# Optimization experiments

Hardware: AMD Instinct MI355X
Metric: run time of the kernel (lower is better)

## Reference

```python
import jax, jax.numpy as jnp
import numpy as np

BETA = 8.0  # cfg.memory.beta (inverse temperature)
EPS = 1e-12  # matches F.normalize default eps


def _l2_normalize(x):
    return x / jnp.maximum(jnp.linalg.norm(x, axis=-1, keepdims=True), EPS)


def setup_inputs() -> dict:
    key = jax.random.key(0)
    k1, k2, k3 = jax.random.split(key, 3)
    embeddings = jax.random.normal(k1, (1024, 128), dtype=jnp.float32)   # queries [B, D]
    keys = jax.random.normal(k2, (100000, 128), dtype=jnp.float32)       # stored patterns [N, D]
    labels = jax.random.randint(k3, (100000,), 0, 1000)                  # class per stored pattern [N]
    return {"embeddings": embeddings, "keys": keys, "labels": labels, "n_classes": 1000}


def reference(embeddings, keys, labels, n_classes):
    # store(): keys normalized (normalize_keys=True); values = one_hot(labels)
    k = _l2_normalize(keys)
    # query(): normalize queries, cosine sims, softmax(beta*sims), weighted value sum
    q = _l2_normalize(embeddings)
    sims = q @ k.T                                   # [B, N]
    weights = jax.nn.softmax(BETA * sims, axis=-1)   # [B, N]
    # weights @ one_hot(labels, C) == segment-sum of weights by key label (same math,
    # avoids materializing the dense [N, C] one-hot value matrix)
    out = jax.ops.segment_sum(weights.T, labels, num_segments=n_classes).T  # [B, C]
    return out
```

## Files before the change

kernel.cpp:

```cpp
#include <hip/hip_runtime.h>
#include <math.h>

typedef _Float16 f16;
typedef _Float16 f16x8 __attribute__((ext_vector_type(8)));
typedef float    f32x16 __attribute__((ext_vector_type(16)));
typedef unsigned int uint;
typedef unsigned short u16;

#define B_Q     1024
#define DIM     128
#define N_KEYS  100000
#define NPAD    102400
#define NGP     (NPAD / 32)
#define GPC     8
#define NCHUNK  (NGP / GPC)
#define N_CLS   1000
#define QSCALE  11.541560327111707f
#define CSUM    10
#define NCB     (N_CLS / CSUM)
#define NH      128

__global__ void k_hist(const int* __restrict__ labels, uint* __restrict__ hist128) {
    __shared__ uint lh[N_CLS];
    for (int i = threadIdx.x; i < N_CLS; i += blockDim.x) lh[i] = 0;
    __syncthreads();
    const int stride = gridDim.x * blockDim.x;
    for (int i = blockIdx.x * blockDim.x + threadIdx.x; i < N_KEYS; i += stride)
        atomicAdd(&lh[labels[i]], 1u);
    __syncthreads();
    for (int i = threadIdx.x; i < N_CLS; i += blockDim.x)
        hist128[blockIdx.x * N_CLS + i] = lh[i];
}

__global__ void k_scan(const uint* __restrict__ hist128, uint* __restrict__ cursor) {
    __shared__ uint s[1024];
    const int t = threadIdx.x;
    uint v = 0;
    if (t < N_CLS)
        for (int b = 0; b < NH; ++b) v += hist128[b * N_CLS + t];
    s[t] = v; __syncthreads();
    for (int o = 1; o < 1024; o <<= 1) {
        const uint x = (t >= o) ? s[t - o] : 0u;
        __syncthreads();
        s[t] += x;
        __syncthreads();
    }
    if (t < N_CLS) cursor[t] = s[t] - v;
}

__global__ void k_prep(const float* __restrict__ qm, const float* __restrict__ km,
                       const int* __restrict__ labels, uint* __restrict__ cursor,
                       f16* __restrict__ kf2, f16* __restrict__ qf2,
                       u16* __restrict__ kcls) {
    const int gid  = blockIdx.x * blockDim.x + threadIdx.x;
    const int n    = gid >> 6;
    const int lane = threadIdx.x & 63;
    if (n >= NPAD + B_Q) return;
    const bool isq   = n >= NPAD;
    const bool dummy = !isq && n >= N_KEYS;

    float a = 0.0f, b = 0.0f;
    if (!dummy) {
        const float* row = isq ? qm + (size_t)(n - NPAD) * DIM
                               : km + (size_t)n * DIM;
        a = row[lane]; b = row[lane + 64];
    }
    float ss = a * a + b * b;
    #pragma unroll
    for (int o = 32; o >= 1; o >>= 1) ss += __shfl_xor(ss, o);
    const float rn = (isq ? QSCALE : 1.0f) / fmaxf(sqrtf(ss), 1e-12f);

    int pos;
    if (isq)        pos = n - NPAD;
    else if (dummy) { pos = n; if (lane == 0) kcls[pos] = (u16)N_CLS; }
    else {
        const int lab = labels[n];
        if (lane == 0) pos = (int)atomicAdd(&cursor[lab], 1u);
        pos = __shfl(pos, 0);
        if (lane == 0) kcls[pos] = (u16)lab;
    }

    const float va = a * rn, vb = b * rn;
    f16x8 hv;
    #pragma unroll
    for (int j = 0; j < 8; ++j) {
        const int src = (lane & 15) * 8 + j;
        const float xa = __shfl(va, src & 63);
        const float xb = __shfl(vb, src & 63);
        hv[j] = (f16)((src < 64) ? xa : xb);
    }
    if (lane < 16) {
        f16* dst = isq ? qf2 : kf2;
        const int kk  = lane >> 1;
        const int lhi = lane & 1;
        *(f16x8*)(dst + (size_t)(pos >> 5) * 4096 + kk * 512 +
                  ((lhi << 5) + (pos & 31)) * 8) = hv;
    }
}

__global__ void k_meta(const u16* __restrict__ kcls, int* __restrict__ meta,
                       float* __restrict__ out_t) {
    const int nt = gridDim.x * blockDim.x;
    const float4 z = {0.0f, 0.0f, 0.0f, 0.0f};
    for (int i = blockIdx.x * blockDim.x + threadIdx.x;
         i < N_CLS * B_Q / 4; i += nt)
        ((float4*)out_t)[i] = z;

    const int gid  = blockIdx.x * blockDim.x + threadIdx.x;
    const int g    = gid >> 6;
    const int lane = threadIdx.x & 63;
    if (g >= NGP) return;
    const int  cl = kcls[g * 32 + (lane & 31)];
    const int  ca = __shfl(cl, 0);
    const uint dm = (uint)(__ballot(cl != ca) & 0xffffffffull);
    const int  split = dm ? (__ffs(dm) - 1) : 32;
    const int  cb = (split < 32) ? __shfl(cl, split) : ca;
    if (lane == 0) meta[g] = ca | (cb << 11) | (split << 22);
}

#define FLUSH2(C) {                                                           \
        const float v0 = racc0 + __shfl_xor(racc0, 32);                       \
        const float v1 = racc1 + __shfl_xor(racc1, 32);                       \
        if (lhi == 0) {                                                       \
            atomicAdd(&out_t[(size_t)(C) * B_Q + q00 + l31], v0);             \
            atomicAdd(&out_t[(size_t)(C) * B_Q + q01 + l31], v1);             \
        }                                                                     \
    }

__global__ __launch_bounds__(256, 3)
void class_gemm6(const f16* __restrict__ kf2, const f16* __restrict__ qf2,
                 const int* __restrict__ meta, float* __restrict__ out_t) {
    const int tid  = threadIdx.x;
    const int w    = tid >> 6;
    const int lane = tid & 63;
    const int l31  = lane & 31;
    const int lhi  = lane >> 5;
    const int lhi4 = lhi << 2;

    const int b     = blockIdx.x;
    const int xcd   = b & 7;
    const int s     = b >> 3;
    const int chunk = xcd * (NCHUNK / 8) + (s >> 2);
    const int qquad = s & 3;
    const int g0    = chunk * GPC;

    f16x8 Q0[8], Q1[8];
    {
        const f16* qa = qf2 + (size_t)(qquad * 8 + w * 2) * 4096 + lane * 8;
        #pragma unroll
        for (int kk = 0; kk < 8; ++kk) {
            Q0[kk] = *(const f16x8*)(qa + kk * 512);
            Q1[kk] = *(const f16x8*)(qa + 4096 + kk * 512);
        }
    }
    const int q00 = qquad * 256 + w * 64;
    const int q01 = q00 + 32;

    const int mv = meta[g0 + (lane & (GPC - 1))];

    float racc0 = 0.0f, racc1 = 0.0f;
    int cur = -1;

    for (int i = 0; i < GPC; ++i) {
        const int m     = __shfl(mv, i);
        const int ca    = m & 0x7FF;
        const int cb    = (m >> 11) & 0x7FF;
        const int split = m >> 22;

        const f16* base = kf2 + (size_t)(g0 + i) * 4096 + lane * 8;
        f32x16 c0 = {}, c1 = {};
        #pragma unroll
        for (int kk = 0; kk < 8; ++kk) {
            const f16x8 Kf = *(const f16x8*)(base + kk * 512);
            c0 = __builtin_amdgcn_mfma_f32_32x32x16_f16(Kf, Q0[kk], c0, 0, 0, 0);
            c1 = __builtin_amdgcn_mfma_f32_32x32x16_f16(Kf, Q1[kk], c1, 0, 0, 0);
        }

        if (ca != cur) {
            if (cur >= 0) FLUSH2(cur);
            racc0 = 0.0f; racc1 = 0.0f;
            cur = ca;
        }
        if (split == 32) {
            float ga = 0.0f, gb = 0.0f, gc = 0.0f, gd = 0.0f;
            #pragma unroll
            for (int r = 0; r < 16; r += 2) {
                ga += __builtin_amdgcn_exp2f(c0[r]);
                gb += __builtin_amdgcn_exp2f(c0[r + 1]);
                gc += __builtin_amdgcn_exp2f(c1[r]);
                gd += __builtin_amdgcn_exp2f(c1[r + 1]);
            }
            racc0 += ga + gb;
            racc1 += gc + gd;
        } else {
            float ga = 0.0f, gb = 0.0f, gc = 0.0f, gd = 0.0f;
            float ha = 0.0f, hb = 0.0f, hc = 0.0f, hd = 0.0f;
            #pragma unroll
            for (int r = 0; r < 16; r += 2) {
                const int  kr0 = ((r & 3) + 8 * (r >> 2)) + lhi4;
                const int  kr1 = (((r + 1) & 3) + 8 * ((r + 1) >> 2)) + lhi4;
                const float e0  = __builtin_amdgcn_exp2f(c0[r]);
                const float e0b = __builtin_amdgcn_exp2f(c0[r + 1]);
                const float e1  = __builtin_amdgcn_exp2f(c1[r]);
                const float e1b = __builtin_amdgcn_exp2f(c1[r + 1]);
                const bool inA0 = kr0 < split;
                const bool inA1 = kr1 < split;
                ga += inA0 ? e0  : 0.0f;  ha += inA0 ? 0.0f : e0;
                gb += inA1 ? e0b : 0.0f;  hb += inA1 ? 0.0f : e0b;
                gc += inA0 ? e1  : 0.0f;  hc += inA0 ? 0.0f : e1;
                gd += inA1 ? e1b : 0.0f;  hd += inA1 ? 0.0f : e1b;
            }
            racc0 += ga + gb;
            racc1 += gc + gd;
            FLUSH2(cur);
            racc0 = ha + hb;
            racc1 = hc + hd;
            cur = cb;
        }
    }
    if (cur >= 0) FLUSH2(cur);
}

__global__ __launch_bounds__(1024)
void k_qsum(const float* __restrict__ out_t, float* __restrict__ partial) {
    const int cb = blockIdx.x;
    const int q  = threadIdx.x;
    const float* p = out_t + (size_t)cb * CSUM * B_Q + q;
    float s = 0.0f;
    #pragma unroll
    for (int i = 0; i < CSUM; ++i) s += p[(size_t)i * B_Q];
    partial[cb * B_Q + q] = s;
}

__global__ __launch_bounds__(256)
void k_norm_t(const float* __restrict__ out_t, const float* __restrict__ partial,
              float* __restrict__ out) {
    __shared__ float tile[64 * 65];
    __shared__ float invq[64];
    const int tid  = threadIdx.x;
    const int w    = tid >> 6;
    const int lane = tid & 63;
    const int q0   = blockIdx.x * 64;
    const int c0   = blockIdx.y * 64;

    if (tid < 64) {
        float s = 0.0f;
        for (int cb = 0; cb < NCB; ++cb) s += partial[cb * B_Q + q0 + tid];
        invq[tid] = 1.0f / s;
    }
    #pragma unroll
    for (int i = 0; i < 16; ++i) {
        const int cidx = c0 + w * 16 + i;
        const float v = (cidx < N_CLS) ? out_t[(size_t)cidx * B_Q + q0 + lane] : 0.0f;
        tile[lane * 65 + w * 16 + i] = v;
    }
    __syncthreads();
    #pragma unroll
    for (int j = 0; j < 16; ++j) {
        const int r    = w * 16 + j;
        const int cidx = c0 + lane;
        if (cidx < N_CLS)
            out[(size_t)(q0 + r) * N_CLS + cidx] = tile[r * 65 + lane] * invq[r];
    }
}

extern "C" void kernel_launch(void* const* d_in, const int* in_sizes, int n_in,
                              void* d_out, int out_size, void* d_ws, size_t ws_size,
                              hipStream_t stream) {
    const float* qm     = (const float*)d_in[0];
    const float* km     = (const float*)d_in[1];
    const int*   labels = (const int*)d_in[2];
    float* out = (float*)d_out;

    char* p = (char*)d_ws;
    f16*   kf2     = (f16*)p;   p += (size_t)NPAD * DIM * 2;
    f16*   qf2     = (f16*)p;   p += (size_t)B_Q * DIM * 2;
    float* out_t   = (float*)p; p += (size_t)N_CLS * B_Q * 4;
    float* partial = (float*)p; p += (size_t)NCB * B_Q * 4;
    uint*  cursor  = (uint*)p;  p += N_CLS * 4;
    u16*   kcls    = (u16*)p;   p += (size_t)NPAD * 2;
    int*   meta    = (int*)p;   p += (size_t)NGP * 4;
    uint*  hist128 = (uint*)out_t;

    hipLaunchKernelGGL(k_hist, dim3(NH), dim3(256), 0, stream, labels, hist128);
    hipLaunchKernelGGL(k_scan, dim3(1), dim3(1024), 0, stream, hist128, cursor);

    const int prows = NPAD + B_Q;
    hipLaunchKernelGGL(k_prep, dim3((prows * 64 + 255) / 256), dim3(256), 0, stream,
                       qm, km, labels, cursor, kf2, qf2, kcls);
    hipLaunchKernelGGL(k_meta, dim3((NGP * 64 + 255) / 256), dim3(256), 0, stream,
                       kcls, meta, out_t);

    hipLaunchKernelGGL(class_gemm6, dim3(4 * NCHUNK), dim3(256), 0, stream,
                       kf2, qf2, meta, out_t);

    hipLaunchKernelGGL(k_qsum, dim3(NCB), dim3(1024), 0, stream, out_t, partial);
    hipLaunchKernelGGL(k_norm_t, dim3(B_Q / 64, (N_CLS + 63) / 64), dim3(256), 0, stream,
                       out_t, partial, out);
}
```

Before: 114.1 us.

## Split key prep into permutation pass and gather kernel writing contiguous tiles

Replaces the one-wavefront-per-row prep kernel, which scattered each normalized row to its sorted position, with two kernels. The first computes the sorted destination for each key with atomics and records a source index. The second gathers 32 source rows per block, normalizes them with a shared-memory reduction, and writes whole fp16 tiles contiguously with vector loads. This removes the cross-lane shuffles and scattered 16-byte writes, and fills every lane. In exchange it adds a kernel launch, an index array round trip, and reads key rows in permuted order.

```diff
diff --git a/kernel.cpp b/kernel.cpp
--- a/kernel.cpp
+++ b/kernel.cpp
@@ -19,6 +19,7 @@
 #define CSUM    10
 #define NCB     (N_CLS / CSUM)
 #define NH      128
+#define QGRP    (B_Q / 32)
 
 __global__ void k_hist(const int* __restrict__ labels, uint* __restrict__ hist128) {
     __shared__ uint lh[N_CLS];
@@ -48,54 +49,78 @@
     if (t < N_CLS) cursor[t] = s[t] - v;
 }
 
-__global__ void k_prep(const float* __restrict__ qm, const float* __restrict__ km,
-                       const int* __restrict__ labels, uint* __restrict__ cursor,
-                       f16* __restrict__ kf2, f16* __restrict__ qf2,
-                       u16* __restrict__ kcls) {
-    const int gid  = blockIdx.x * blockDim.x + threadIdx.x;
-    const int n    = gid >> 6;
-    const int lane = threadIdx.x & 63;
-    if (n >= NPAD + B_Q) return;
-    const bool isq   = n >= NPAD;
-    const bool dummy = !isq && n >= N_KEYS;
-
-    float a = 0.0f, b = 0.0f;
-    if (!dummy) {
-        const float* row = isq ? qm + (size_t)(n - NPAD) * DIM
-                               : km + (size_t)n * DIM;
-        a = row[lane]; b = row[lane + 64];
-    }
-    float ss = a * a + b * b;
-    #pragma unroll
-    for (int o = 32; o >= 1; o >>= 1) ss += __shfl_xor(ss, o);
-    const float rn = (isq ? QSCALE : 1.0f) / fmaxf(sqrtf(ss), 1e-12f);
-
-    int pos;
-    if (isq)        pos = n - NPAD;
-    else if (dummy) { pos = n; if (lane == 0) kcls[pos] = (u16)N_CLS; }
+__global__ void k_perm(const int* __restrict__ labels, uint* __restrict__ cursor,
+                       int* __restrict__ src, u16* __restrict__ kcls) {
+    const int n = blockIdx.x * blockDim.x + threadIdx.x;
+    if (n >= NPAD) return;
+    if (n < N_KEYS) {
+        const int lab = labels[n];
+        const int pos = (int)atomicAdd(&cursor[lab], 1u);
+        src[pos]  = n;
+        kcls[pos] = (u16)lab;
+    } else {
+        src[n]  = -1;
+        kcls[n] = (u16)N_CLS;
+    }
+}
+
+__global__ __launch_bounds__(256)
+void k_gather(const float* __restrict__ qm, const float* __restrict__ km,
+              const int* __restrict__ src, f16* __restrict__ kf2,
+              f16* __restrict__ qf2) {
+    __shared__ float ssq[8][32];
+    __shared__ float scale[32];
+    const int g = blockIdx.x;
+    const int t = threadIdx.x;
+    const int r = t & 31;
+    const int p = t >> 5;
+    const bool isq = g >= NGP;
+
+    const float* srow;
+    if (isq) srow = qm + (size_t)((g - NGP) * 32 + r) * DIM;
     else {
-        const int lab = labels[n];
-        if (lane == 0) pos = (int)atomicAdd(&cursor[lab], 1u);
-        pos = __shfl(pos, 0);
-        if (lane == 0) kcls[pos] = (u16)lab;
-    }
-
-    const float va = a * rn, vb = b * rn;
-    f16x8 hv;
+        const int sr = src[g * 32 + r];
+        srow = (sr >= 0) ? km + (size_t)sr * DIM : nullptr;
+    }
+
+    float4 v[4];
+    float ss = 0.0f;
+    if (srow) {
+        #pragma unroll
+        for (int i = 0; i < 4; ++i) {
+            v[i] = *(const float4*)(srow + p * 16 + i * 4);
+            ss += v[i].x * v[i].x + v[i].y * v[i].y
+                + v[i].z * v[i].z + v[i].w * v[i].w;
+        }
+    } else {
+        #pragma unroll
+        for (int i = 0; i < 4; ++i) v[i] = float4{0.f, 0.f, 0.f, 0.f};
+    }
+    ssq[p][r] = ss;
+    __syncthreads();
+    if (t < 32) {
+        float s = 0.0f;
+        #pragma unroll
+        for (int i = 0; i < 8; ++i) s += ssq[i][t];
+        scale[t] = (isq ? QSCALE : 1.0f) / fmaxf(sqrtf(s), 1e-12f);
+    }
+    __syncthreads();
+    const float sc = scale[r];
+
+    const float f[16] = {v[0].x, v[0].y, v[0].z, v[0].w,
+                         v[1].x, v[1].y, v[1].z, v[1].w,
+                         v[2].x, v[2].y, v[2].z, v[2].w,
+                         v[3].x, v[3].y, v[3].z, v[3].w};
+    f16x8 h0, h1;
     #pragma unroll
     for (int j = 0; j < 8; ++j) {
-        const int src = (lane & 15) * 8 + j;
-        const float xa = __shfl(va, src & 63);
-        const float xb = __shfl(vb, src & 63);
-        hv[j] = (f16)((src < 64) ? xa : xb);
-    }
-    if (lane < 16) {
-        f16* dst = isq ? qf2 : kf2;
-        const int kk  = lane >> 1;
-        const int lhi = lane & 1;
-        *(f16x8*)(dst + (size_t)(pos >> 5) * 4096 + kk * 512 +
-                  ((lhi << 5) + (pos & 31)) * 8) = hv;
-    }
+        h0[j] = (f16)(f[j]     * sc);
+        h1[j] = (f16)(f[j + 8] * sc);
+    }
+    f16* dst = isq ? qf2 + (size_t)(g - NGP) * 4096
+                   : kf2 + (size_t)g * 4096;
+    *(f16x8*)(dst + p * 512 +       r * 8) = h0;
+    *(f16x8*)(dst + p * 512 + 256 + r * 8) = h1;
 }
 
 __global__ void k_meta(const u16* __restrict__ kcls, int* __restrict__ meta,
@@ -280,14 +305,15 @@
     uint*  cursor  = (uint*)p;  p += N_CLS * 4;
     u16*   kcls    = (u16*)p;   p += (size_t)NPAD * 2;
     int*   meta    = (int*)p;   p += (size_t)NGP * 4;
+    int*   src     = (int*)p;   p += (size_t)NPAD * 4;
     uint*  hist128 = (uint*)out_t;
 
     hipLaunchKernelGGL(k_hist, dim3(NH), dim3(256), 0, stream, labels, hist128);
     hipLaunchKernelGGL(k_scan, dim3(1), dim3(1024), 0, stream, hist128, cursor);
-
-    const int prows = NPAD + B_Q;
-    hipLaunchKernelGGL(k_prep, dim3((prows * 64 + 255) / 256), dim3(256), 0, stream,
-                       qm, km, labels, cursor, kf2, qf2, kcls);
+    hipLaunchKernelGGL(k_perm, dim3(NPAD / 256), dim3(256), 0, stream,
+                       labels, cursor, src, kcls);
+    hipLaunchKernelGGL(k_gather, dim3(NGP + QGRP), dim3(256), 0, stream,
+                       qm, km, src, kf2, qf2);
     hipLaunchKernelGGL(k_meta, dim3((NGP * 64 + 255) / 256), dim3(256), 0, stream,
                        kcls, meta, out_t);
 
```

Measured after the change: 110.7 us. 3.0% less time.
